# Kernel tuning notes

Hardware: AMD Instinct MI355X
Metric: run time of the kernel (lower is better)

## Reference

```python
import jax, jax.numpy as jnp
import numpy as np

EPS = 1e-7  # K.epsilon()


def setup_inputs() -> dict:
    key = jax.random.key(0)
    k1, k2, k3 = jax.random.split(key, 3)
    B, T, D = 64, 2048, 256
    x = jax.random.normal(k1, (B, T, D), dtype=jnp.float32)
    W = jax.random.normal(k2, (D, D), dtype=jnp.float32) * (1.0 / np.sqrt(D))
    b = jnp.zeros((D,), dtype=jnp.float32)
    uw = jax.random.normal(k3, (D,), dtype=jnp.float32) * (1.0 / np.sqrt(D))
    mask = jnp.ones((B, T), dtype=jnp.int32)
    return {"x": x, "W": W, "b": b, "uw": uw, "mask": mask}


def reference(x, W, b, uw, mask):
    # x: [B, T, D]; W: [D, D]; b, uw: [D]; mask: [B, T]
    eij = jnp.tanh(jnp.einsum('btd,de->bte', x, W) + b)   # [B, T, D]
    eij = jnp.einsum('btd,d->bt', eij, uw)                # [B, T]
    a = jnp.exp(eij) * mask.astype(x.dtype)               # [B, T]
    a = a / (jnp.sum(a, axis=1, keepdims=True) + EPS)     # normalize over time
    return jnp.einsum('btd,bt->bd', x, a)                 # [B, D]
```

## Files before the change

kernel.cpp:

```cpp
#include <hip/hip_runtime.h>
#include <hip/hip_bf16.h>

#define BB 64
#define TT 2048
#define DD 256
#define EPSF 1e-7f
#define XS_STRIDE 264

typedef __attribute__((ext_vector_type(8))) short v8s;
typedef __attribute__((ext_vector_type(4))) float v4f;

__device__ __forceinline__ float bf2f(unsigned short u) {
    union { unsigned int i; float f; } c;
    c.i = ((unsigned int)u) << 16;
    return c.f;
}

__device__ __forceinline__ unsigned int pack2_bf16(float a, float b) {
    union { __hip_bfloat162 h; unsigned int u; } c;
    c.h = __float22bfloat162_rn(make_float2(a, b));
    return c.u;
}

__device__ __forceinline__ float tanh_fast(float x) {
    float e = __expf(2.0f * x);
    return 1.0f - 2.0f / (e + 1.0f);
}

__global__ __launch_bounds__(256) void pack_wt(const float* __restrict__ W,
                                               unsigned short* __restrict__ Wt) {
    __shared__ float tile[32][33];
    int bx = blockIdx.x & 7;
    int by = blockIdx.x >> 3;
    int r  = threadIdx.x >> 3;
    int c4 = (threadIdx.x & 7) * 4;
    float4 v = *(const float4*)(W + (size_t)(bx * 32 + r) * DD + by * 32 + c4);
    tile[r][c4 + 0] = v.x; tile[r][c4 + 1] = v.y;
    tile[r][c4 + 2] = v.z; tile[r][c4 + 3] = v.w;
    __syncthreads();
    float a0 = tile[c4 + 0][r], a1 = tile[c4 + 1][r];
    float a2 = tile[c4 + 2][r], a3 = tile[c4 + 3][r];
    uint2 pp = make_uint2(pack2_bf16(a0, a1), pack2_bf16(a2, a3));
    *(uint2*)(Wt + (size_t)(by * 32 + r) * DD + bx * 32 + c4) = pp;
}

__global__ __launch_bounds__(256) void fused_att(const float* __restrict__ x,
                                                 const unsigned short* __restrict__ Wt,
                                                 const float* __restrict__ bias,
                                                 const float* __restrict__ uw,
                                                 const int* __restrict__ mask,
                                                 float* __restrict__ numpart,
                                                 float* __restrict__ denpart) {
    __shared__ unsigned short xs[64 * XS_STRIDE];
    __shared__ float ered[4][64];
    __shared__ float pshared[64];

    const int tid  = threadIdx.x;
    const int wave = tid >> 6;
    const int lane = tid & 63;
    const int quad = lane >> 4;
    const int m    = lane & 15;
    const long rowbase = (long)blockIdx.x * 64;

    float bias_r[4], uw_r[4];
#pragma unroll
    for (int i = 0; i < 4; ++i) {
        int n = (wave * 4 + i) * 16 + m;
        bias_r[i] = bias[n];
        uw_r[i]   = uw[n];
    }

    {
        const float* gp = x + (rowbase + wave * 16) * (long)DD + lane * 4;
        unsigned short* sp = xs + (size_t)(wave * 16) * XS_STRIDE + lane * 4;
#pragma unroll
        for (int r = 0; r < 16; ++r) {
            float4 v = *(const float4*)(gp + (long)r * DD);
            uint2 pp = make_uint2(pack2_bf16(v.x, v.y), pack2_bf16(v.z, v.w));
            *(uint2*)(sp + (size_t)r * XS_STRIDE) = pp;
        }
    }
    __syncthreads();

    float esum[4][4];
#pragma unroll
    for (int mt = 0; mt < 4; ++mt)
#pragma unroll
        for (int r = 0; r < 4; ++r) esum[mt][r] = 0.f;

#pragma unroll
    for (int i = 0; i < 4; ++i) {
        const int nt = wave * 4 + i;
        const unsigned short* bp = Wt + (size_t)(nt * 16 + m) * DD + quad * 8;
        v8s bfrag[8];
#pragma unroll
        for (int ks = 0; ks < 8; ++ks) bfrag[ks] = *(const v8s*)(bp + ks * 32);
#pragma unroll
        for (int mt = 0; mt < 4; ++mt) {
            const unsigned short* ap = xs + (size_t)(mt * 16 + m) * XS_STRIDE + quad * 8;
            v4f acc = {0.f, 0.f, 0.f, 0.f};
#pragma unroll
            for (int ks = 0; ks < 8; ++ks) {
                v8s af = *(const v8s*)(ap + ks * 32);
                acc = __builtin_amdgcn_mfma_f32_16x16x32_bf16(af, bfrag[ks], acc, 0, 0, 0);
            }
#pragma unroll
            for (int r = 0; r < 4; ++r)
                esum[mt][r] += tanh_fast(acc[r] + bias_r[i]) * uw_r[i];
        }
    }

#pragma unroll
    for (int o = 1; o < 16; o <<= 1)
#pragma unroll
        for (int mt = 0; mt < 4; ++mt)
#pragma unroll
            for (int r = 0; r < 4; ++r)
                esum[mt][r] += __shfl_xor(esum[mt][r], o, 64);
    if (m == 0) {
#pragma unroll
        for (int mt = 0; mt < 4; ++mt)
#pragma unroll
            for (int r = 0; r < 4; ++r)
                ered[wave][mt * 16 + quad * 4 + r] = esum[mt][r];
    }
    __syncthreads();

    if (tid < 64) {
        float e = ered[0][tid] + ered[1][tid] + ered[2][tid] + ered[3][tid];
        float p = __expf(e) * (float)mask[rowbase + tid];
        pshared[tid] = p;
        float s = p;
#pragma unroll
        for (int o = 1; o < 64; o <<= 1) s += __shfl_xor(s, o, 64);
        if (tid == 0) denpart[blockIdx.x] = s;
    }
    __syncthreads();

    float num = 0.f;
#pragma unroll 8
    for (int t = 0; t < 64; ++t) {
        num += pshared[t] * bf2f(xs[(size_t)t * XS_STRIDE + tid]);
    }
    numpart[(size_t)blockIdx.x * DD + tid] = num;
}

__global__ __launch_bounds__(256) void finalize(const float* __restrict__ numpart,
                                                const float* __restrict__ denpart,
                                                float* __restrict__ out) {
    __shared__ float dsh;
    int b = blockIdx.x, d = threadIdx.x;
    if (d == 0) {
        float s = 0.f;
        for (int c = 0; c < 32; ++c) s += denpart[b * 32 + c];
        dsh = s + EPSF;
    }
    __syncthreads();
    float s = 0.f;
#pragma unroll
    for (int c = 0; c < 32; ++c) s += numpart[(size_t)(b * 32 + c) * DD + d];
    out[(size_t)b * DD + d] = s / dsh;
}

extern "C" void kernel_launch(void* const* d_in, const int* in_sizes, int n_in,
                              void* d_out, int out_size, void* d_ws, size_t ws_size,
                              hipStream_t stream) {
    const float* x    = (const float*)d_in[0];
    const float* W    = (const float*)d_in[1];
    const float* bias = (const float*)d_in[2];
    const float* uw   = (const float*)d_in[3];
    const int*   mask = (const int*)d_in[4];
    float*       out  = (float*)d_out;

    char* ws = (char*)d_ws;
    unsigned short* Wt = (unsigned short*)ws;
    float* numpart     = (float*)(ws + 131072);
    float* denpart     = (float*)(ws + 131072 + 2097152);

    pack_wt<<<dim3(64), dim3(256), 0, stream>>>(W, Wt);
    fused_att<<<dim3(2048), dim3(256), 0, stream>>>(x, Wt, bias, uw, mask, numpart, denpart);
    finalize<<<dim3(64), dim3(256), 0, stream>>>(numpart, denpart, out);
}
```

Before: 233.8 us.

## Give each wave its own 16 rows to drop block barriers in attention kernel

```diff
diff --git a/kernel.cpp b/kernel.cpp
--- a/kernel.cpp
+++ b/kernel.cpp
@@ -44,105 +44,106 @@
     *(uint2*)(Wt + (size_t)(by * 32 + r) * DD + bx * 32 + c4) = pp;
 }
 
-__global__ __launch_bounds__(256) void fused_att(const float* __restrict__ x,
-                                                 const unsigned short* __restrict__ Wt,
-                                                 const float* __restrict__ bias,
-                                                 const float* __restrict__ uw,
-                                                 const int* __restrict__ mask,
-                                                 float* __restrict__ numpart,
-                                                 float* __restrict__ denpart) {
-    __shared__ unsigned short xs[64 * XS_STRIDE];
-    __shared__ float ered[4][64];
-    __shared__ float pshared[64];
+__global__ __launch_bounds__(256) void fused_att2(const float* __restrict__ x,
+                                                  const unsigned short* __restrict__ Wt,
+                                                  const float* __restrict__ bias,
+                                                  const float* __restrict__ uw,
+                                                  const int* __restrict__ mask,
+                                                  float* __restrict__ numpart,
+                                                  float* __restrict__ denpart) {
+    __shared__ unsigned short xs[4 * 16 * XS_STRIDE];
+    __shared__ float red[4][DD];
+    __shared__ float denred[4];
 
     const int tid  = threadIdx.x;
-    const int wave = tid >> 6;
+    const int w    = tid >> 6;
     const int lane = tid & 63;
     const int quad = lane >> 4;
     const int m    = lane & 15;
-    const long rowbase = (long)blockIdx.x * 64;
+    const long R0  = (long)blockIdx.x * 64 + w * 16;
 
-    float bias_r[4], uw_r[4];
-#pragma unroll
-    for (int i = 0; i < 4; ++i) {
-        int n = (wave * 4 + i) * 16 + m;
-        bias_r[i] = bias[n];
-        uw_r[i]   = uw[n];
+    unsigned short* xw = xs + (size_t)w * 16 * XS_STRIDE;
+
+    {
+        const float* gp = x + R0 * DD + lane * 4;
+#pragma unroll 8
+        for (int r = 0; r < 16; ++r) {
+            float4 v = *(const float4*)(gp + (size_t)r * DD);
+            uint2 pp = make_uint2(pack2_bf16(v.x, v.y), pack2_bf16(v.z, v.w));
+            *(uint2*)(xw + (size_t)r * XS_STRIDE + lane * 4) = pp;
+        }
     }
 
+    v8s afrag[8];
     {
-        const float* gp = x + (rowbase + wave * 16) * (long)DD + lane * 4;
-        unsigned short* sp = xs + (size_t)(wave * 16) * XS_STRIDE + lane * 4;
+        const unsigned short* ap = xw + (size_t)m * XS_STRIDE + quad * 8;
 #pragma unroll
-        for (int r = 0; r < 16; ++r) {
-            float4 v = *(const float4*)(gp + (long)r * DD);
-            uint2 pp = make_uint2(pack2_bf16(v.x, v.y), pack2_bf16(v.z, v.w));
-            *(uint2*)(sp + (size_t)r * XS_STRIDE) = pp;
-        }
+        for (int ks = 0; ks < 8; ++ks) afrag[ks] = *(const v8s*)(ap + ks * 32);
     }
-    __syncthreads();
 
-    float esum[4][4];
-#pragma unroll
-    for (int mt = 0; mt < 4; ++mt)
-#pragma unroll
-        for (int r = 0; r < 4; ++r) esum[mt][r] = 0.f;
-
-#pragma unroll
-    for (int i = 0; i < 4; ++i) {
-        const int nt = wave * 4 + i;
-        const unsigned short* bp = Wt + (size_t)(nt * 16 + m) * DD + quad * 8;
+    float esum[4] = {0.f, 0.f, 0.f, 0.f};
+#pragma unroll 2
+    for (int nt = 0; nt < 16; ++nt) {
+        const int n = nt * 16 + m;
+        const unsigned short* bp = Wt + (size_t)n * DD + quad * 8;
         v8s bfrag[8];
 #pragma unroll
         for (int ks = 0; ks < 8; ++ks) bfrag[ks] = *(const v8s*)(bp + ks * 32);
+        v4f acc = {0.f, 0.f, 0.f, 0.f};
 #pragma unroll
-        for (int mt = 0; mt < 4; ++mt) {
-            const unsigned short* ap = xs + (size_t)(mt * 16 + m) * XS_STRIDE + quad * 8;
-            v4f acc = {0.f, 0.f, 0.f, 0.f};
+        for (int ks = 0; ks < 8; ++ks)
+            acc = __builtin_amdgcn_mfma_f32_16x16x32_bf16(afrag[ks], bfrag[ks], acc, 0, 0, 0);
+        const float bb = bias[n];
+        const float un = uw[n];
 #pragma unroll
-            for (int ks = 0; ks < 8; ++ks) {
-                v8s af = *(const v8s*)(ap + ks * 32);
-                acc = __builtin_amdgcn_mfma_f32_16x16x32_bf16(af, bfrag[ks], acc, 0, 0, 0);
-            }
-#pragma unroll
-            for (int r = 0; r < 4; ++r)
-                esum[mt][r] += tanh_fast(acc[r] + bias_r[i]) * uw_r[i];
-        }
+        for (int r = 0; r < 4; ++r)
+            esum[r] += tanh_fast(acc[r] + bb) * un;
     }
 
 #pragma unroll
     for (int o = 1; o < 16; o <<= 1)
 #pragma unroll
-        for (int mt = 0; mt < 4; ++mt)
+        for (int r = 0; r < 4; ++r)
+            esum[r] += __shfl_xor(esum[r], o, 64);
+
+    const int4 mv = *(const int4*)(mask + R0 + quad * 4);
+    float pr[4];
+    pr[0] = __expf(esum[0]) * (float)mv.x;
+    pr[1] = __expf(esum[1]) * (float)mv.y;
+    pr[2] = __expf(esum[2]) * (float)mv.z;
+    pr[3] = __expf(esum[3]) * (float)mv.w;
+
+    float p_all[16];
 #pragma unroll
-            for (int r = 0; r < 4; ++r)
-                esum[mt][r] += __shfl_xor(esum[mt][r], o, 64);
-    if (m == 0) {
+    for (int q = 0; q < 4; ++q)
 #pragma unroll
-        for (int mt = 0; mt < 4; ++mt)
+        for (int r = 0; r < 4; ++r)
+            p_all[q * 4 + r] = __shfl(pr[r], q * 16 + m, 64);
+
+    float den = 0.f;
 #pragma unroll
-            for (int r = 0; r < 4; ++r)
-                ered[wave][mt * 16 + quad * 4 + r] = esum[mt][r];
+    for (int t = 0; t < 16; ++t) den += p_all[t];
+
+    float num[4] = {0.f, 0.f, 0.f, 0.f};
+    {
+        const unsigned short* xp = xw + lane * 4;
+#pragma unroll
+        for (int t = 0; t < 16; ++t) {
+            uint2 xv = *(const uint2*)(xp + (size_t)t * XS_STRIDE);
+            float pt = p_all[t];
+            num[0] += pt * bf2f((unsigned short)(xv.x & 0xffffu));
+            num[1] += pt * bf2f((unsigned short)(xv.x >> 16));
+            num[2] += pt * bf2f((unsigned short)(xv.y & 0xffffu));
+            num[3] += pt * bf2f((unsigned short)(xv.y >> 16));
+        }
     }
+
+    *(float4*)&red[w][lane * 4] = make_float4(num[0], num[1], num[2], num[3]);
+    if (lane == 0) denred[w] = den;
     __syncthreads();
-
-    if (tid < 64) {
-        float e = ered[0][tid] + ered[1][tid] + ered[2][tid] + ered[3][tid];
-        float p = __expf(e) * (float)mask[rowbase + tid];
-        pshared[tid] = p;
-        float s = p;
-#pragma unroll
-        for (int o = 1; o < 64; o <<= 1) s += __shfl_xor(s, o, 64);
-        if (tid == 0) denpart[blockIdx.x] = s;
-    }
-    __syncthreads();
-
-    float num = 0.f;
-#pragma unroll 8
-    for (int t = 0; t < 64; ++t) {
-        num += pshared[t] * bf2f(xs[(size_t)t * XS_STRIDE + tid]);
-    }
-    numpart[(size_t)blockIdx.x * DD + tid] = num;
+    float s = red[0][tid] + red[1][tid] + red[2][tid] + red[3][tid];
+    numpart[(size_t)blockIdx.x * DD + tid] = s;
+    if (tid == 0) denpart[blockIdx.x] = denred[0] + denred[1] + denred[2] + denred[3] ;
 }
 
 __global__ __launch_bounds__(256) void finalize(const float* __restrict__ numpart,
@@ -178,6 +179,6 @@
     float* denpart     = (float*)(ws + 131072 + 2097152);
 
     pack_wt<<<dim3(64), dim3(256), 0, stream>>>(W, Wt);
-    fused_att<<<dim3(2048), dim3(256), 0, stream>>>(x, Wt, bias, uw, mask, numpart, denpart);
+    fused_att2<<<dim3(2048), dim3(256), 0, stream>>>(x, Wt, bias, uw, mask, numpart, denpart);
     finalize<<<dim3(64), dim3(256), 0, stream>>>(numpart, denpart, out);
 }
```

New measurement: 306.5 us. 31.1% more time.

## Restructure MFMA loop with A-fragment reuse, B double-buffering and per-wave pooling

Applied to the files above, without the earlier changes.

```diff
diff --git a/kernel.cpp b/kernel.cpp
--- a/kernel.cpp
+++ b/kernel.cpp
@@ -44,38 +44,39 @@
     *(uint2*)(Wt + (size_t)(by * 32 + r) * DD + bx * 32 + c4) = pp;
 }
 
-__global__ __launch_bounds__(256) void fused_att(const float* __restrict__ x,
-                                                 const unsigned short* __restrict__ Wt,
-                                                 const float* __restrict__ bias,
-                                                 const float* __restrict__ uw,
-                                                 const int* __restrict__ mask,
-                                                 float* __restrict__ numpart,
-                                                 float* __restrict__ denpart) {
+__global__ __launch_bounds__(256, 3) void fused_att3(const float* __restrict__ x,
+                                                     const unsigned short* __restrict__ Wt,
+                                                     const float* __restrict__ bias,
+                                                     const float* __restrict__ uw,
+                                                     const int* __restrict__ mask,
+                                                     float* __restrict__ numpart,
+                                                     float* __restrict__ denpart) {
     __shared__ unsigned short xs[64 * XS_STRIDE];
     __shared__ float ered[4][64];
-    __shared__ float pshared[64];
+    __shared__ float red[4][DD];
+    __shared__ float denred[4];
 
     const int tid  = threadIdx.x;
-    const int wave = tid >> 6;
+    const int w    = tid >> 6;
     const int lane = tid & 63;
     const int quad = lane >> 4;
     const int m    = lane & 15;
-    const long rowbase = (long)blockIdx.x * 64;
+    const long R0  = (long)blockIdx.x * 64 + w * 16;
 
     float bias_r[4], uw_r[4];
 #pragma unroll
     for (int i = 0; i < 4; ++i) {
-        int n = (wave * 4 + i) * 16 + m;
+        int n = (w * 4 + i) * 16 + m;
         bias_r[i] = bias[n];
         uw_r[i]   = uw[n];
     }
 
     {
-        const float* gp = x + (rowbase + wave * 16) * (long)DD + lane * 4;
-        unsigned short* sp = xs + (size_t)(wave * 16) * XS_STRIDE + lane * 4;
-#pragma unroll
+        const float* gp = x + R0 * DD + lane * 4;
+        unsigned short* sp = xs + (size_t)(w * 16) * XS_STRIDE + lane * 4;
+#pragma unroll 8
         for (int r = 0; r < 16; ++r) {
-            float4 v = *(const float4*)(gp + (long)r * DD);
+            float4 v = *(const float4*)(gp + (size_t)r * DD);
             uint2 pp = make_uint2(pack2_bf16(v.x, v.y), pack2_bf16(v.z, v.w));
             *(uint2*)(sp + (size_t)r * XS_STRIDE) = pp;
         }
@@ -89,24 +90,42 @@
         for (int r = 0; r < 4; ++r) esum[mt][r] = 0.f;
 
 #pragma unroll
-    for (int i = 0; i < 4; ++i) {
-        const int nt = wave * 4 + i;
-        const unsigned short* bp = Wt + (size_t)(nt * 16 + m) * DD + quad * 8;
-        v8s bfrag[8];
-#pragma unroll
-        for (int ks = 0; ks < 8; ++ks) bfrag[ks] = *(const v8s*)(bp + ks * 32);
-#pragma unroll
-        for (int mt = 0; mt < 4; ++mt) {
-            const unsigned short* ap = xs + (size_t)(mt * 16 + m) * XS_STRIDE + quad * 8;
-            v4f acc = {0.f, 0.f, 0.f, 0.f};
+    for (int h = 0; h < 2; ++h) {
+        v8s a0[8], a1[8];
+        {
+            const unsigned short* ap0 = xs + (size_t)(2 * h * 16 + m) * XS_STRIDE + quad * 8;
 #pragma unroll
             for (int ks = 0; ks < 8; ++ks) {
-                v8s af = *(const v8s*)(ap + ks * 32);
-                acc = __builtin_amdgcn_mfma_f32_16x16x32_bf16(af, bfrag[ks], acc, 0, 0, 0);
-            }
-#pragma unroll
-            for (int r = 0; r < 4; ++r)
-                esum[mt][r] += tanh_fast(acc[r] + bias_r[i]) * uw_r[i];
+                a0[ks] = *(const v8s*)(ap0 + ks * 32);
+                a1[ks] = *(const v8s*)(ap0 + 16 * XS_STRIDE + ks * 32);
+            }
+        }
+        v8s bbuf[2][8];
+        {
+            const unsigned short* bp = Wt + (size_t)(w * 4 * 16 + m) * DD + quad * 8;
+#pragma unroll
+            for (int ks = 0; ks < 8; ++ks) bbuf[0][ks] = *(const v8s*)(bp + ks * 32);
+        }
+#pragma unroll
+        for (int i = 0; i < 4; ++i) {
+            const int cur = i & 1;
+            if (i < 3) {
+                const unsigned short* bp = Wt + (size_t)((w * 4 + i + 1) * 16 + m) * DD + quad * 8;
+#pragma unroll
+                for (int ks = 0; ks < 8; ++ks) bbuf[cur ^ 1][ks] = *(const v8s*)(bp + ks * 32);
+            }
+            v4f acc0 = {0.f, 0.f, 0.f, 0.f};
+            v4f acc1 = {0.f, 0.f, 0.f, 0.f};
+#pragma unroll
+            for (int ks = 0; ks < 8; ++ks) {
+                acc0 = __builtin_amdgcn_mfma_f32_16x16x32_bf16(a0[ks], bbuf[cur][ks], acc0, 0, 0, 0);
+                acc1 = __builtin_amdgcn_mfma_f32_16x16x32_bf16(a1[ks], bbuf[cur][ks], acc1, 0, 0, 0);
+            }
+#pragma unroll
+            for (int r = 0; r < 4; ++r) {
+                esum[2 * h][r]     += tanh_fast(acc0[r] + bias_r[i]) * uw_r[i];
+                esum[2 * h + 1][r] += tanh_fast(acc1[r] + bias_r[i]) * uw_r[i];
+            }
         }
     }
 
@@ -122,27 +141,41 @@
         for (int mt = 0; mt < 4; ++mt)
 #pragma unroll
             for (int r = 0; r < 4; ++r)
-                ered[wave][mt * 16 + quad * 4 + r] = esum[mt][r];
-    }
-    __syncthreads();
-
-    if (tid < 64) {
-        float e = ered[0][tid] + ered[1][tid] + ered[2][tid] + ered[3][tid];
-        float p = __expf(e) * (float)mask[rowbase + tid];
-        pshared[tid] = p;
-        float s = p;
-#pragma unroll
-        for (int o = 1; o < 64; o <<= 1) s += __shfl_xor(s, o, 64);
-        if (tid == 0) denpart[blockIdx.x] = s;
-    }
-    __syncthreads();
-
-    float num = 0.f;
-#pragma unroll 8
-    for (int t = 0; t < 64; ++t) {
-        num += pshared[t] * bf2f(xs[(size_t)t * XS_STRIDE + tid]);
-    }
-    numpart[(size_t)blockIdx.x * DD + tid] = num;
+                ered[w][mt * 16 + quad * 4 + r] = esum[mt][r];
+    }
+    __syncthreads();
+
+    const int rl = lane & 15;
+    float et = ered[0][w * 16 + rl] + ered[1][w * 16 + rl]
+             + ered[2][w * 16 + rl] + ered[3][w * 16 + rl];
+    float p_loc = __expf(et) * (float)mask[R0 + rl];
+    float p_all[16];
+#pragma unroll
+    for (int t = 0; t < 16; ++t) p_all[t] = __shfl(p_loc, t, 64);
+    float den = 0.f;
+#pragma unroll
+    for (int t = 0; t < 16; ++t) den += p_all[t];
+
+    float num[4] = {0.f, 0.f, 0.f, 0.f};
+    {
+        const unsigned short* xp = xs + (size_t)(w * 16) * XS_STRIDE + lane * 4;
+#pragma unroll
+        for (int t = 0; t < 16; ++t) {
+            uint2 xv = *(const uint2*)(xp + (size_t)t * XS_STRIDE);
+            float pt = p_all[t];
+            num[0] += pt * bf2f((unsigned short)(xv.x & 0xffffu));
+            num[1] += pt * bf2f((unsigned short)(xv.x >> 16));
+            num[2] += pt * bf2f((unsigned short)(xv.y & 0xffffu));
+            num[3] += pt * bf2f((unsigned short)(xv.y >> 16));
+        }
+    }
+
+    *(float4*)&red[w][lane * 4] = make_float4(num[0], num[1], num[2], num[3]);
+    if (lane == 0) denred[w] = den;
+    __syncthreads();
+    float s = red[0][tid] + red[1][tid] + red[2][tid] + red[3][tid];
+    numpart[(size_t)blockIdx.x * DD + tid] = s;
+    if (tid == 0) denpart[blockIdx.x] = denred[0] + denred[1] + denred[2] + denred[3];
 }
 
 __global__ __launch_bounds__(256) void finalize(const float* __restrict__ numpart,
@@ -178,6 +211,6 @@
     float* denpart     = (float*)(ws + 131072 + 2097152);
 
     pack_wt<<<dim3(64), dim3(256), 0, stream>>>(W, Wt);
-    fused_att<<<dim3(2048), dim3(256), 0, stream>>>(x, Wt, bias, uw, mask, numpart, denpart);
+    fused_att3<<<dim3(2048), dim3(256), 0, stream>>>(x, Wt, bias, uw, mask, numpart, denpart);
     finalize<<<dim3(64), dim3(256), 0, stream>>>(numpart, denpart, out);
 }
```

New measurement: 231.6 us. No clear change (-0.9%).
